# Optimization experiments

Measured on AMD Instinct MI355X. Metric: run time of the kernel, lower is better.

## Reference

```python
import jax, jax.numpy as jnp
import numpy as np
from jax import lax

B, H, S = 256, 256, 512


def setup_inputs() -> dict:
    key = jax.random.key(0)
    ks = jax.random.split(key, 7)
    sc = 1.0 / np.sqrt(H).astype(np.float32)
    tree_state = jax.random.normal(ks[0], (B, H), jnp.float32)
    seq_states = jax.random.normal(ks[1], (B, H, S), jnp.float32)
    seq_mask = jax.random.randint(ks[2], (B, S), 0, 2, jnp.int32)
    W_ih = jax.random.uniform(ks[3], (3 * H, H), jnp.float32, -sc, sc)
    W_hh = jax.random.uniform(ks[4], (3 * H, H), jnp.float32, -sc, sc)
    b_ih = jax.random.uniform(ks[5], (3 * H,), jnp.float32, -sc, sc)
    b_hh = jax.random.uniform(ks[6], (3 * H,), jnp.float32, -sc, sc)
    return {"tree_state": tree_state, "seq_states": seq_states, "seq_mask": seq_mask,
            "W_ih": W_ih, "W_hh": W_hh, "b_ih": b_ih, "b_hh": b_hh}


def _gru_cell(x, h, W_ih, W_hh, b_ih, b_hh):
    # torch.nn.GRUCell math. x, h: (B, H); W_*: (3H, H); b_*: (3H,)
    gi = x @ W_ih.T + b_ih          # (B, 3H)
    gh = h @ W_hh.T + b_hh          # (B, 3H)
    i_r, i_z, i_n = jnp.split(gi, 3, axis=-1)
    h_r, h_z, h_n = jnp.split(gh, 3, axis=-1)
    r = jax.nn.sigmoid(i_r + h_r)
    z = jax.nn.sigmoid(i_z + h_z)
    n = jnp.tanh(i_n + r * h_n)
    return (1.0 - z) * n + z * h


def reference(tree_state, seq_states, seq_mask, W_ih, W_hh, b_ih, b_hh):
    # sequential recurrent scan over the seq axis of seq_states (batch, hid, seq)
    xs = jnp.transpose(seq_states, (2, 0, 1))  # (S, B, H)

    def step(h, x):
        h_new = _gru_cell(x, h, W_ih, W_hh, b_ih, b_hh)
        return h_new, h_new

    _, outs = lax.scan(step, tree_state, xs)      # (S, B, H)
    rnn_out = jnp.transpose(outs, (1, 0, 2))      # (B, S, H)
    # get_final_encoder_states: last unmasked timestep per row
    last_idx = jnp.maximum(jnp.sum(seq_mask, axis=1) - 1, 0)  # (B,)
    final = jnp.take_along_axis(rnn_out, last_idx[:, None, None], axis=1)  # (B,1,H)
    return final[:, 0, :]
```

## Files before the change

### kernel.cpp

```cpp
#include <hip/hip_runtime.h>
#include <hip/hip_bf16.h>

#define HH 256
#define SSL 512
#define G3 768

using short8 = __attribute__((ext_vector_type(8))) short;
using f32x4  = __attribute__((ext_vector_type(4))) float;

__device__ __forceinline__ unsigned short f2bf(float f) {
  unsigned int u = __float_as_uint(f);
  u += 0x7FFFu + ((u >> 16) & 1u);
  return (unsigned short)(u >> 16);
}
__device__ __forceinline__ float bf2f(unsigned short b) {
  return __uint_as_float(((unsigned int)b) << 16);
}
__device__ __forceinline__ void block_sync_lds() {
  asm volatile("s_waitcnt lgkmcnt(0)\n\ts_barrier" ::: "memory");
}

__global__ __launch_bounds__(256) void prep_pack(
    const float* __restrict__ Wih, const float* __restrict__ Whh,
    unsigned short* __restrict__ wih_bf, unsigned short* __restrict__ whh_frag)
{
  int blk = blockIdx.x;
  if (blk < 96) {
    int base = (blk * 256 + threadIdx.x) * 4;
#pragma unroll
    for (int i = 0; i < 4; i++) {
      int u = base + i;
      float a = Wih[2 * u], b = Wih[2 * u + 1];
      ((unsigned int*)wih_bf)[u] = (unsigned int)f2bf(a) | ((unsigned int)f2bf(b) << 16);
    }
  } else {
    int gid = (blk - 96) * 256 + threadIdx.x;
    int f = gid >> 6, l = gid & 63;
    int kt = f & 7, mt = (f >> 3) & 1, g = (f >> 4) % 3, w = f / 48;
    int row = g * HH + w * 32 + mt * 16 + (l & 15);
    int k0  = kt * 32 + (l >> 4) * 8;
    const float* src = Whh + (size_t)row * HH + k0;
    unsigned int o[4];
#pragma unroll
    for (int i = 0; i < 4; i++)
      o[i] = (unsigned int)f2bf(src[2 * i]) | ((unsigned int)f2bf(src[2 * i + 1]) << 16);
    *(uint4*)(whh_frag + ((size_t)f * 64 + l) * 8) = *(uint4*)o;
  }
}

__global__ __launch_bounds__(512, 4) void gi_gemm(
    const float* __restrict__ X, const unsigned short* __restrict__ Wb,
    const float* __restrict__ bih, unsigned short* __restrict__ gi)
{
  __shared__ __align__(16) char smem[36864];
  unsigned short* Al = (unsigned short*)smem;
  unsigned short* Bl = (unsigned short*)(smem + 16384);
  float (*Dl)[132] = (float(*)[132])smem;

  const int tid  = threadIdx.x;
  const int lane = tid & 63;
  const int wave = tid >> 6;
  const int wm   = wave >> 2;
  const int wj   = wave & 3;
  const int n16  = lane & 15;
  const int quad = lane >> 4;

  const int mblk = blockIdx.y;
  const int b    = mblk >> 2;
  const int s0   = (mblk & 3) * 128;
  const int j0   = blockIdx.x * 128;

  f32x4 acc[4][2];
#pragma unroll
  for (int mt = 0; mt < 4; mt++)
#pragma unroll
    for (int jt = 0; jt < 2; jt++) acc[mt][jt] = f32x4{0.f, 0.f, 0.f, 0.f};

  const float* Xb = X + (size_t)b * (HH * SSL);

  float4 xa[2][2];
  uint4  wbv[2];

  auto ldA = [&](int kt, int q, float4* dst) {
    int idx = tid + 512 * q, sq = idx & 31, a = idx >> 5;
    const float* p = Xb + (size_t)(kt * 64 + 2 * a) * SSL + s0 + 4 * sq;
    dst[0] = *(const float4*)p;
    dst[1] = *(const float4*)(p + SSL);
  };
  auto ldB = [&](int kt, int q) -> uint4 {
    int cid = tid + 512 * q, j = cid >> 3, c = cid & 7;
    return *(const uint4*)(Wb + (size_t)(j0 + j) * HH + kt * 64 + c * 8);
  };

  ldA(0, 0, xa[0]); ldA(0, 1, xa[1]);
  wbv[0] = ldB(0, 0); wbv[1] = ldB(0, 1);

  for (int kt = 0; kt < 4; kt++) {
#pragma unroll
    for (int q = 0; q < 2; q++) {
      int idx = tid + 512 * q, sq = idx & 31, a = idx >> 5;
      int c = a >> 2, d = a & 3;
#pragma unroll
      for (int r = 0; r < 4; r++) {
        int s = 4 * sq + r;
        int sw = (s + (s >> 3)) & 7;
        unsigned int u =
            (unsigned int)f2bf(((const float*)&xa[q][0])[r]) |
            ((unsigned int)f2bf(((const float*)&xa[q][1])[r]) << 16);
        *(unsigned int*)(Al + s * 64 + ((c ^ sw) * 8) + d * 2) = u;
      }
    }
#pragma unroll
    for (int p = 0; p < 2; p++) {
      int cid = tid + 512 * p, j = cid >> 3, c = cid & 7;
      int sw = (j + (j >> 3)) & 7;
      *(uint4*)(Bl + j * 64 + ((c ^ sw) * 8)) = wbv[p];
    }
    __syncthreads();
    if (kt < 3) {
      ldA(kt + 1, 0, xa[0]); ldA(kt + 1, 1, xa[1]);
      wbv[0] = ldB(kt + 1, 0); wbv[1] = ldB(kt + 1, 1);
    }
#pragma unroll
    for (int kk = 0; kk < 2; kk++) {
      short8 af[4], bfr[2];
#pragma unroll
      for (int mt = 0; mt < 4; mt++) {
        int s = wm * 64 + mt * 16 + n16;
        int sw = (s + (s >> 3)) & 7;
        af[mt] = *(const short8*)(Al + s * 64 + (((kk * 4 + quad) ^ sw) * 8));
      }
#pragma unroll
      for (int jt = 0; jt < 2; jt++) {
        int j = wj * 32 + jt * 16 + n16;
        int sw = (j + (j >> 3)) & 7;
        bfr[jt] = *(const short8*)(Bl + j * 64 + (((kk * 4 + quad) ^ sw) * 8));
      }
#pragma unroll
      for (int mt = 0; mt < 4; mt++)
#pragma unroll
        for (int jt = 0; jt < 2; jt++)
          acc[mt][jt] = __builtin_amdgcn_mfma_f32_16x16x32_bf16(af[mt], bfr[jt], acc[mt][jt], 0, 0, 0);
    }
    __syncthreads();
  }

  float bias[2];
  bias[0] = bih[j0 + wj * 32 + 0 * 16 + n16];
  bias[1] = bih[j0 + wj * 32 + 1 * 16 + n16];

  for (int c = 0; c < 2; c++) {
    __syncthreads();
    if (wm == c) {
#pragma unroll
      for (int mt = 0; mt < 4; mt++)
#pragma unroll
        for (int jt = 0; jt < 2; jt++)
#pragma unroll
          for (int r = 0; r < 4; r++)
            Dl[mt * 16 + quad * 4 + r][wj * 32 + jt * 16 + n16] = acc[mt][jt][r] + bias[jt];
    }
    __syncthreads();
#pragma unroll
    for (int i = 0; i < 2; i++) {
      int ml = (tid >> 4) + 32 * i;
      int jj = (tid & 15) * 8;
      float4 p0 = *(const float4*)&Dl[ml][jj];
      float4 p1 = *(const float4*)&Dl[ml][jj + 4];
      short8 st;
      st[0] = (short)f2bf(p0.x); st[1] = (short)f2bf(p0.y);
      st[2] = (short)f2bf(p0.z); st[3] = (short)f2bf(p0.w);
      st[4] = (short)f2bf(p1.x); st[5] = (short)f2bf(p1.y);
      st[6] = (short)f2bf(p1.z); st[7] = (short)f2bf(p1.w);
      int sgl = s0 + c * 64 + ml;
      *(short8*)(gi + ((size_t)b * SSL + sgl) * G3 + j0 + jj) = st;
    }
  }
}

__global__ __launch_bounds__(512, 1) void gru_scan(
    const float* __restrict__ tree, const int* __restrict__ mask,
    const unsigned short* __restrict__ wfrag, const float* __restrict__ bhh,
    const unsigned short* __restrict__ gi, float* __restrict__ out)
{
  __shared__ __align__(16) unsigned char lds[86016];
  unsigned short* wlds = (unsigned short*)lds;
  unsigned short (*hfrag)[8][4][4][8] =
      (unsigned short(*)[8][4][4][8])(lds + 49152);
  float* preF = (float*)(lds + 53248);
  int*   lsum = (int*)(lds + 65920);

  const int tid  = threadIdx.x;
  const int lane = tid & 63;
  const int w    = tid >> 6;
  const int n16  = lane & 15;
  const int quad = lane >> 4;
  const int brow0 = blockIdx.x * 4;
  const int bb = tid >> 7;
  const int jj = (tid & 127) * 2;

  if (tid < 4) lsum[tid] = 0;
#pragma unroll
  for (int i = 0; i < 6; i++) {
    int cid = tid + 512 * i;
    int l = cid & 63, rest = cid >> 6;
    int ktp = rest % 3, mtp = (rest / 3) & 1, wp = rest / 6;
    int F = ((wp * 3 + 2) * 2 + mtp) * 8 + (5 + ktp);
    uint4 v = *(const uint4*)(wfrag + ((size_t)F * 64 + l) * 8);
    *(uint4*)(wlds + (((size_t)(wp * 2 + mtp) * 3 + ktp) * 64 + l) * 8) = v;
  }
  __syncthreads();
  {
    const int* mp = mask + (size_t)(brow0 + bb) * SSL + (tid & 127) * 4;
    atomicAdd(&lsum[bb], mp[0] + mp[1] + mp[2] + mp[3]);
  }

  short8 aw[2][2][8];
#pragma unroll
  for (int g = 0; g < 2; g++)
#pragma unroll
    for (int mt = 0; mt < 2; mt++)
#pragma unroll
      for (int kt = 0; kt < 8; kt++) {
        int F = ((w * 3 + g) * 2 + mt) * 8 + kt;
        aw[g][mt][kt] = *(const short8*)(wfrag + ((size_t)F * 64 + lane) * 8);
      }
  short8 aw2[2][5];
#pragma unroll
  for (int mt = 0; mt < 2; mt++)
#pragma unroll
    for (int kt = 0; kt < 5; kt++) {
      int F = ((w * 3 + 2) * 2 + mt) * 8 + kt;
      aw2[mt][kt] = *(const short8*)(wfrag + ((size_t)F * 64 + lane) * 8);
    }
#pragma unroll
  for (int g = 0; g < 2; g++)
#pragma unroll
    for (int mt = 0; mt < 2; mt++)
#pragma unroll
      for (int kt = 0; kt < 8; kt++)
        asm volatile("" : "+v"(aw[g][mt][kt]));
#pragma unroll
  for (int mt = 0; mt < 2; mt++)
#pragma unroll
    for (int kt = 0; kt < 5; kt++)
      asm volatile("" : "+v"(aw2[mt][kt]));

  float bhr0 = bhh[jj],        bhr1 = bhh[jj + 1];
  float bhz0 = bhh[HH + jj],   bhz1 = bhh[HH + jj + 1];
  float bhn0 = bhh[2*HH + jj], bhn1 = bhh[2*HH + jj + 1];

  float h0 = tree[(size_t)(brow0 + bb) * HH + jj];
  float h1 = tree[(size_t)(brow0 + bb) * HH + jj + 1];
  *(unsigned int*)&hfrag[0][jj >> 5][bb][(jj >> 3) & 3][jj & 7] =
      (unsigned int)f2bf(h0) | ((unsigned int)f2bf(h1) << 16);
  __syncthreads();
  int last = lsum[bb] - 1; if (last < 0) last = 0;

  const unsigned short* gib = gi + (size_t)(brow0 + bb) * SSL * G3;
  unsigned int giA[3], giB[3];
#pragma unroll
  for (int g = 0; g < 3; g++) giA[g] = *(const unsigned int*)(gib + (size_t)0 * G3 + g * HH + jj);
#pragma unroll
  for (int g = 0; g < 3; g++) giB[g] = *(const unsigned int*)(gib + (size_t)1 * G3 + g * HH + jj);

  auto step = [&](int t, unsigned int* gv) {
    const int cb = t & 1, nb = cb ^ 1;
    float gir0 = bf2f((unsigned short)(gv[0] & 0xFFFF)), gir1 = bf2f((unsigned short)(gv[0] >> 16));
    float giz0 = bf2f((unsigned short)(gv[1] & 0xFFFF)), giz1 = bf2f((unsigned short)(gv[1] >> 16));
    float gin0 = bf2f((unsigned short)(gv[2] & 0xFFFF)), gin1 = bf2f((unsigned short)(gv[2] >> 16));

    f32x4 acc[3][2];
#pragma unroll
    for (int g = 0; g < 3; g++)
#pragma unroll
      for (int mt = 0; mt < 2; mt++) acc[g][mt] = f32x4{0.f, 0.f, 0.f, 0.f};
#pragma unroll
    for (int kt = 0; kt < 8; kt++) {
      short8 hb = *(const short8*)&hfrag[cb][kt][n16 & 3][quad][0];
#pragma unroll
      for (int mt = 0; mt < 2; mt++) {
        acc[0][mt] = __builtin_amdgcn_mfma_f32_16x16x32_bf16(aw[0][mt][kt], hb, acc[0][mt], 0, 0, 0);
        acc[1][mt] = __builtin_amdgcn_mfma_f32_16x16x32_bf16(aw[1][mt][kt], hb, acc[1][mt], 0, 0, 0);
        short8 w2 = (kt < 5) ? aw2[mt][kt]
                  : *(const short8*)(wlds + (((size_t)(w * 2 + mt) * 3 + (kt - 5)) * 64 + lane) * 8);
        acc[2][mt] = __builtin_amdgcn_mfma_f32_16x16x32_bf16(w2, hb, acc[2][mt], 0, 0, 0);
      }
    }
    if (n16 < 4) {
#pragma unroll
      for (int g = 0; g < 3; g++)
#pragma unroll
        for (int mt = 0; mt < 2; mt++)
          *(f32x4*)(preF + g * 1056 + n16 * 264 + w * 32 + mt * 16 + quad * 4) = acc[g][mt];
    }
    int tn = (t + 2 < SSL) ? t + 2 : SSL - 1;
    gv[0] = *(const unsigned int*)(gib + (size_t)tn * G3 + 0 * HH + jj);
    gv[1] = *(const unsigned int*)(gib + (size_t)tn * G3 + 1 * HH + jj);
    gv[2] = *(const unsigned int*)(gib + (size_t)tn * G3 + 2 * HH + jj);
    block_sync_lds();

    float2 pr = *(const float2*)(preF + 0 * 1056 + bb * 264 + jj);
    float2 pz = *(const float2*)(preF + 1 * 1056 + bb * 264 + jj);
    float2 pn = *(const float2*)(preF + 2 * 1056 + bb * 264 + jj);
    float hr0 = pr.x + bhr0 + gir0, hr1 = pr.y + bhr1 + gir1;
    float hz0 = pz.x + bhz0 + giz0, hz1 = pz.y + bhz1 + giz1;
    float hn0 = pn.x + bhn0,        hn1 = pn.y + bhn1;
    float r0 = __builtin_amdgcn_rcpf(1.f + __expf(-hr0));
    float r1 = __builtin_amdgcn_rcpf(1.f + __expf(-hr1));
    float z0 = __builtin_amdgcn_rcpf(1.f + __expf(-hz0));
    float z1 = __builtin_amdgcn_rcpf(1.f + __expf(-hz1));
    float a0 = gin0 + r0 * hn0, a1 = gin1 + r1 * hn1;
    float nn0 = 1.f - 2.f * __builtin_amdgcn_rcpf(__expf(2.f * a0) + 1.f);
    float nn1 = 1.f - 2.f * __builtin_amdgcn_rcpf(__expf(2.f * a1) + 1.f);
    float hN0 = nn0 + z0 * (h0 - nn0);
    float hN1 = nn1 + z1 * (h1 - nn1);
    h0 = hN0; h1 = hN1;
    *(unsigned int*)&hfrag[nb][jj >> 5][bb][(jj >> 3) & 3][jj & 7] =
        (unsigned int)f2bf(hN0) | ((unsigned int)f2bf(hN1) << 16);
    if (t == last) {
      out[(size_t)(brow0 + bb) * HH + jj] = hN0;
      out[(size_t)(brow0 + bb) * HH + jj + 1] = hN1;
    }
    block_sync_lds();
  };

  for (int t = 0; t < SSL; t += 2) {
    step(t, giA);
    step(t + 1, giB);
  }
}

extern "C" void kernel_launch(void* const* d_in, const int* in_sizes, int n_in,
                              void* d_out, int out_size, void* d_ws, size_t ws_size,
                              hipStream_t stream) {
  const float* tree = (const float*)d_in[0];
  const float* seq  = (const float*)d_in[1];
  const int*   mask = (const int*)d_in[2];
  const float* Wih  = (const float*)d_in[3];
  const float* Whh  = (const float*)d_in[4];
  const float* bih  = (const float*)d_in[5];
  const float* bhh  = (const float*)d_in[6];
  float* out = (float*)d_out;

  unsigned short* gi      = (unsigned short*)d_ws;
  unsigned short* wih_bf  = (unsigned short*)((char*)d_ws + 201326592);
  unsigned short* whh_frag= (unsigned short*)((char*)d_ws + 201719808);

  prep_pack<<<192, 256, 0, stream>>>(Wih, Whh, wih_bf, whh_frag);
  gi_gemm<<<dim3(6, 1024), 512, 0, stream>>>(seq, wih_bf, bih, gi);
  gru_scan<<<64, 512, 0, stream>>>(tree, mask, whh_frag, bhh, gi, out);
}
```

Before: 1.021 ms.

## Pin recurrent weights in AGPRs, fold r/z hidden biases into GEMM, restructure MFMA loop

The r and z hidden biases (b_hh) are folded into the bias of the input-projection GEMM, so the scan step does fewer adds. In the scan kernel, the register-resident W_hh fragments are pinned to AGPRs instead of VGPRs, and the n-gate split moves from 5 register/3 LDS k-tiles to 4/4, which enlarges the LDS weight buffer. The MFMA loop is reordered per m-tile so only three accumulators are live at once, and launch bounds become (512,2), all to reduce register pressure. The risk is that AGPR operands or extra LDS reads for the n-gate weights lengthen the serial per-step critical path. Folding the biases before the bf16 rounding of gi also slightly changes rounding.

After: 1.002 ms. Within noise of the previous version (-1.9%).

```diff
diff --git a/kernel.cpp b/kernel.cpp
--- a/kernel.cpp
+++ b/kernel.cpp
@@ -50,7 +50,8 @@
 
 __global__ __launch_bounds__(512, 4) void gi_gemm(
     const float* __restrict__ X, const unsigned short* __restrict__ Wb,
-    const float* __restrict__ bih, unsigned short* __restrict__ gi)
+    const float* __restrict__ bih, const float* __restrict__ bhh,
+    unsigned short* __restrict__ gi)
 {
   __shared__ __align__(16) char smem[36864];
   unsigned short* Al = (unsigned short*)smem;
@@ -146,8 +147,12 @@
   }
 
   float bias[2];
-  bias[0] = bih[j0 + wj * 32 + 0 * 16 + n16];
-  bias[1] = bih[j0 + wj * 32 + 1 * 16 + n16];
+  {
+    int jg0 = j0 + wj * 32 + 0 * 16 + n16;
+    int jg1 = j0 + wj * 32 + 1 * 16 + n16;
+    bias[0] = bih[jg0] + (jg0 < 2 * HH ? bhh[jg0] : 0.f);
+    bias[1] = bih[jg1] + (jg1 < 2 * HH ? bhh[jg1] : 0.f);
+  }
 
   for (int c = 0; c < 2; c++) {
     __syncthreads();
@@ -178,17 +183,17 @@
   }
 }
 
-__global__ __launch_bounds__(512, 1) void gru_scan(
+__global__ __launch_bounds__(512, 2) void gru_scan(
     const float* __restrict__ tree, const int* __restrict__ mask,
     const unsigned short* __restrict__ wfrag, const float* __restrict__ bhh,
     const unsigned short* __restrict__ gi, float* __restrict__ out)
 {
-  __shared__ __align__(16) unsigned char lds[86016];
+  __shared__ __align__(16) unsigned char lds[82432];
   unsigned short* wlds = (unsigned short*)lds;
   unsigned short (*hfrag)[8][4][4][8] =
-      (unsigned short(*)[8][4][4][8])(lds + 49152);
-  float* preF = (float*)(lds + 53248);
-  int*   lsum = (int*)(lds + 65920);
+      (unsigned short(*)[8][4][4][8])(lds + 65536);
+  float* preF = (float*)(lds + 69632);
+  int*   lsum = (int*)(lds + 82304);
 
   const int tid  = threadIdx.x;
   const int lane = tid & 63;
@@ -201,13 +206,13 @@
 
   if (tid < 4) lsum[tid] = 0;
 #pragma unroll
-  for (int i = 0; i < 6; i++) {
+  for (int i = 0; i < 8; i++) {
     int cid = tid + 512 * i;
     int l = cid & 63, rest = cid >> 6;
-    int ktp = rest % 3, mtp = (rest / 3) & 1, wp = rest / 6;
-    int F = ((wp * 3 + 2) * 2 + mtp) * 8 + (5 + ktp);
+    int ktp = rest & 3, mtp = (rest >> 2) & 1, wp = rest >> 3;
+    int F = ((wp * 3 + 2) * 2 + mtp) * 8 + (4 + ktp);
     uint4 v = *(const uint4*)(wfrag + ((size_t)F * 64 + l) * 8);
-    *(uint4*)(wlds + (((size_t)(wp * 2 + mtp) * 3 + ktp) * 64 + l) * 8) = v;
+    *(uint4*)(wlds + (((size_t)((wp * 2 + mtp) * 4 + ktp)) * 64 + l) * 8) = v;
   }
   __syncthreads();
   {
@@ -225,13 +230,13 @@
         int F = ((w * 3 + g) * 2 + mt) * 8 + kt;
         aw[g][mt][kt] = *(const short8*)(wfrag + ((size_t)F * 64 + lane) * 8);
       }
-  short8 aw2[2][5];
+  short8 awC[2][4];
 #pragma unroll
   for (int mt = 0; mt < 2; mt++)
 #pragma unroll
-    for (int kt = 0; kt < 5; kt++) {
+    for (int kt = 0; kt < 4; kt++) {
       int F = ((w * 3 + 2) * 2 + mt) * 8 + kt;
-      aw2[mt][kt] = *(const short8*)(wfrag + ((size_t)F * 64 + lane) * 8);
+      awC[mt][kt] = *(const short8*)(wfrag + ((size_t)F * 64 + lane) * 8);
     }
 #pragma unroll
   for (int g = 0; g < 2; g++)
@@ -239,16 +244,14 @@
     for (int mt = 0; mt < 2; mt++)
 #pragma unroll
       for (int kt = 0; kt < 8; kt++)
-        asm volatile("" : "+v"(aw[g][mt][kt]));
+        asm volatile("" : "+a"(aw[g][mt][kt]));
 #pragma unroll
   for (int mt = 0; mt < 2; mt++)
 #pragma unroll
-    for (int kt = 0; kt < 5; kt++)
-      asm volatile("" : "+v"(aw2[mt][kt]));
-
-  float bhr0 = bhh[jj],        bhr1 = bhh[jj + 1];
-  float bhz0 = bhh[HH + jj],   bhz1 = bhh[HH + jj + 1];
-  float bhn0 = bhh[2*HH + jj], bhn1 = bhh[2*HH + jj + 1];
+    for (int kt = 0; kt < 4; kt++)
+      asm volatile("" : "+a"(awC[mt][kt]));
+
+  float bhn0 = bhh[2 * HH + jj], bhn1 = bhh[2 * HH + jj + 1];
 
   float h0 = tree[(size_t)(brow0 + bb) * HH + jj];
   float h1 = tree[(size_t)(brow0 + bb) * HH + jj + 1];
@@ -270,29 +273,25 @@
     float giz0 = bf2f((unsigned short)(gv[1] & 0xFFFF)), giz1 = bf2f((unsigned short)(gv[1] >> 16));
     float gin0 = bf2f((unsigned short)(gv[2] & 0xFFFF)), gin1 = bf2f((unsigned short)(gv[2] >> 16));
 
-    f32x4 acc[3][2];
-#pragma unroll
-    for (int g = 0; g < 3; g++)
-#pragma unroll
-      for (int mt = 0; mt < 2; mt++) acc[g][mt] = f32x4{0.f, 0.f, 0.f, 0.f};
-#pragma unroll
-    for (int kt = 0; kt < 8; kt++) {
-      short8 hb = *(const short8*)&hfrag[cb][kt][n16 & 3][quad][0];
-#pragma unroll
-      for (int mt = 0; mt < 2; mt++) {
-        acc[0][mt] = __builtin_amdgcn_mfma_f32_16x16x32_bf16(aw[0][mt][kt], hb, acc[0][mt], 0, 0, 0);
-        acc[1][mt] = __builtin_amdgcn_mfma_f32_16x16x32_bf16(aw[1][mt][kt], hb, acc[1][mt], 0, 0, 0);
-        short8 w2 = (kt < 5) ? aw2[mt][kt]
-                  : *(const short8*)(wlds + (((size_t)(w * 2 + mt) * 3 + (kt - 5)) * 64 + lane) * 8);
-        acc[2][mt] = __builtin_amdgcn_mfma_f32_16x16x32_bf16(w2, hb, acc[2][mt], 0, 0, 0);
-      }
-    }
-    if (n16 < 4) {
-#pragma unroll
-      for (int g = 0; g < 3; g++)
-#pragma unroll
-        for (int mt = 0; mt < 2; mt++)
-          *(f32x4*)(preF + g * 1056 + n16 * 264 + w * 32 + mt * 16 + quad * 4) = acc[g][mt];
+#pragma unroll
+    for (int mt = 0; mt < 2; mt++) {
+      f32x4 a0 = f32x4{0.f, 0.f, 0.f, 0.f};
+      f32x4 a1 = f32x4{0.f, 0.f, 0.f, 0.f};
+      f32x4 a2 = f32x4{0.f, 0.f, 0.f, 0.f};
+#pragma unroll
+      for (int kt = 0; kt < 8; kt++) {
+        short8 hb = *(const short8*)&hfrag[cb][kt][n16 & 3][quad][0];
+        a0 = __builtin_amdgcn_mfma_f32_16x16x32_bf16(aw[0][mt][kt], hb, a0, 0, 0, 0);
+        a1 = __builtin_amdgcn_mfma_f32_16x16x32_bf16(aw[1][mt][kt], hb, a1, 0, 0, 0);
+        short8 w2 = (kt < 4) ? awC[mt][kt]
+                  : *(const short8*)(wlds + (((size_t)((w * 2 + mt) * 4 + (kt - 4))) * 64 + lane) * 8);
+        a2 = __builtin_amdgcn_mfma_f32_16x16x32_bf16(w2, hb, a2, 0, 0, 0);
+      }
+      if (n16 < 4) {
+        *(f32x4*)(preF + 0 * 1056 + n16 * 264 + w * 32 + mt * 16 + quad * 4) = a0;
+        *(f32x4*)(preF + 1 * 1056 + n16 * 264 + w * 32 + mt * 16 + quad * 4) = a1;
+        *(f32x4*)(preF + 2 * 1056 + n16 * 264 + w * 32 + mt * 16 + quad * 4) = a2;
+      }
     }
     int tn = (t + 2 < SSL) ? t + 2 : SSL - 1;
     gv[0] = *(const unsigned int*)(gib + (size_t)tn * G3 + 0 * HH + jj);
@@ -303,9 +302,9 @@
     float2 pr = *(const float2*)(preF + 0 * 1056 + bb * 264 + jj);
     float2 pz = *(const float2*)(preF + 1 * 1056 + bb * 264 + jj);
     float2 pn = *(const float2*)(preF + 2 * 1056 + bb * 264 + jj);
-    float hr0 = pr.x + bhr0 + gir0, hr1 = pr.y + bhr1 + gir1;
-    float hz0 = pz.x + bhz0 + giz0, hz1 = pz.y + bhz1 + giz1;
-    float hn0 = pn.x + bhn0,        hn1 = pn.y + bhn1;
+    float hr0 = pr.x + gir0, hr1 = pr.y + gir1;
+    float hz0 = pz.x + giz0, hz1 = pz.y + giz1;
+    float hn0 = pn.x + bhn0, hn1 = pn.y + bhn1;
     float r0 = __builtin_amdgcn_rcpf(1.f + __expf(-hr0));
     float r1 = __builtin_amdgcn_rcpf(1.f + __expf(-hr1));
     float z0 = __builtin_amdgcn_rcpf(1.f + __expf(-hz0));
@@ -348,6 +347,6 @@
   unsigned short* whh_frag= (unsigned short*)((char*)d_ws + 201719808);
 
   prep_pack<<<192, 256, 0, stream>>>(Wih, Whh, wih_bf, whh_frag);
-  gi_gemm<<<dim3(6, 1024), 512, 0, stream>>>(seq, wih_bf, bih, gi);
+  gi_gemm<<<dim3(6, 1024), 512, 0, stream>>>(seq, wih_bf, bih, bhh, gi);
   gru_scan<<<64, 512, 0, stream>>>(tree, mask, whh_frag, bhh, gi, out);
 }
```
